# Kernel optimization log

Measured on AMD Instinct MI355X. Metric: run time of the kernel, lower is better.

The kernel has to match this reference:

```python
import jax, jax.numpy as jnp
import numpy as np
from jax import lax

# Model dims (see init_kwargs / mamba_ssm defaults)
B_, L_, D_IN = 8, 512, 128
D_MODEL, N_LAYERS = 512, 2
EXPAND, D_STATE, D_CONV = 2, 16, 4
D_INNER = EXPAND * D_MODEL          # 1024
DT_RANK = (D_MODEL + 15) // 16      # 32


def setup_inputs() -> dict:
    key = jax.random.key(0)
    ks = iter(jax.random.split(key, 32))
    def p(shape, scale=0.02):
        return jax.random.normal(next(ks), shape, jnp.float32) * scale
    inp = {}
    inp["x"] = jax.random.normal(next(ks), (B_, L_, D_IN), jnp.float32)
    # input projection (Linear(input_dim, d_model), with bias)
    inp["proj_in_w"] = p((D_MODEL, D_IN))
    inp["proj_in_b"] = p((D_MODEL,))
    # stacked per-layer Mamba params (leading dim = N_LAYERS)
    inp["in_proj_w"] = p((N_LAYERS, 2 * D_INNER, D_MODEL))      # no bias (mamba default)
    inp["conv_w"]    = p((N_LAYERS, D_INNER, D_CONV))           # depthwise conv1d
    inp["conv_b"]    = p((N_LAYERS, D_INNER))
    inp["x_proj_w"]  = p((N_LAYERS, DT_RANK + 2 * D_STATE, D_INNER))
    inp["dt_proj_w"] = p((N_LAYERS, D_INNER, DT_RANK))
    inp["dt_proj_b"] = jnp.full((N_LAYERS, D_INNER), 0.1, jnp.float32)
    inp["A_log"]     = jnp.log(jnp.tile(jnp.arange(1, D_STATE + 1, dtype=jnp.float32), (N_LAYERS, D_INNER, 1)))
    inp["Dm"]        = jnp.ones((N_LAYERS, D_INNER), jnp.float32)
    inp["out_proj_w"] = p((N_LAYERS, D_MODEL, D_INNER))         # no bias
    # classifier head: Linear(d_model, 64) -> ReLU -> Linear(64, 1)
    inp["cls_w1"] = p((64, D_MODEL)); inp["cls_b1"] = p((64,))
    inp["cls_w2"] = p((1, 64));       inp["cls_b2"] = p((1,))
    return inp


def _mamba_block(h, in_w, cw, cb, xp_w, dt_w, dt_b, A_log, Dm, out_w):
    B, L, _ = h.shape
    xz = jnp.einsum('bld,ed->ble', h, in_w)           # (B, L, 2*d_inner)
    xi, z = jnp.split(xz, 2, axis=-1)
    # causal depthwise conv1d (pad left d_conv-1, crop to L)
    xc = xi.transpose(0, 2, 1)                         # (B, d_inner, L)
    xc = lax.conv_general_dilated(
        xc, cw[:, None, :], (1,), [(D_CONV - 1, 0)],
        feature_group_count=D_INNER,
        dimension_numbers=('NCH', 'OIH', 'NCH')) + cb[None, :, None]
    xc = jax.nn.silu(xc).transpose(0, 2, 1)            # (B, L, d_inner)
    x_dbl = jnp.einsum('bld,ed->ble', xc, xp_w)        # (B, L, dt_rank + 2*d_state)
    dt, Bm, Cm = jnp.split(x_dbl, [DT_RANK, DT_RANK + D_STATE], axis=-1)
    dt = jax.nn.softplus(jnp.einsum('blr,dr->bld', dt, dt_w) + dt_b)  # (B, L, d_inner)
    A = -jnp.exp(A_log)                                # (d_inner, d_state)

    def step(hst, ins):
        dt_t, B_t, C_t, x_t = ins                      # (B,di),(B,ds),(B,ds),(B,di)
        dA = jnp.exp(dt_t[..., None] * A)              # (B, di, ds)
        hst = dA * hst + (dt_t * x_t)[..., None] * B_t[:, None, :]
        y = jnp.einsum('bds,bs->bd', hst, C_t)
        return hst, y

    h0 = jnp.zeros((B, D_INNER, D_STATE), h.dtype)
    xs = (dt.transpose(1, 0, 2), Bm.transpose(1, 0, 2),
          Cm.transpose(1, 0, 2), xc.transpose(1, 0, 2))
    _, ys = lax.scan(step, h0, xs)                     # ys: (L, B, d_inner)
    y = ys.transpose(1, 0, 2) + xc * Dm                # skip term D*x
    y = y * jax.nn.silu(z)                             # gate
    return jnp.einsum('ble,de->bld', y, out_w)         # (B, L, d_model)


def reference(x, proj_in_w, proj_in_b, in_proj_w, conv_w, conv_b, x_proj_w,
              dt_proj_w, dt_proj_b, A_log, Dm, out_proj_w,
              cls_w1, cls_b1, cls_w2, cls_b2):
    h = jnp.einsum('bli,di->bld', x, proj_in_w) + proj_in_b
    for l in range(N_LAYERS):
        h = _mamba_block(h, in_proj_w[l], conv_w[l], conv_b[l], x_proj_w[l],
                         dt_proj_w[l], dt_proj_b[l], A_log[l], Dm[l], out_proj_w[l])
    h = h.mean(axis=1)                                 # (B, d_model); dropout = identity (eval)
    h = jax.nn.relu(h @ cls_w1.T + cls_b1)
    logits = (h @ cls_w2.T + cls_b2).squeeze(-1)       # (B,)
    return logits
```

## Files before the change

kernel.cpp:

```cpp
#include <hip/hip_runtime.h>
#include <hip/hip_bf16.h>

#define B_   8
#define L_   512
#define DIN  128
#define DM   512
#define NLAY 2
#define DI   1024
#define DS   16
#define DTR  32
#define BL   (B_ * L_)
#define KS   8
#define CL   128
#define NCH  (L_ / CL)

typedef short bf16x8 __attribute__((ext_vector_type(8)));
typedef float floatx4 __attribute__((ext_vector_type(4)));

__device__ __forceinline__ unsigned short f2bf(float f) {
    unsigned int u = __float_as_uint(f);
    unsigned int r = (u + 0x7FFF + ((u >> 16) & 1)) >> 16;
    return (unsigned short)r;
}
__device__ __forceinline__ float bf2f(unsigned short u) {
    return __uint_as_float((unsigned int)u << 16);
}

#if __has_builtin(__builtin_amdgcn_exp2f)
#define EXP2(x) __builtin_amdgcn_exp2f(x)
#else
#define EXP2(x) __expf((x) * 0.69314718056f)
#endif

__device__ __forceinline__ void gld_lds16(const unsigned short* g, unsigned short* l) {
    __builtin_amdgcn_global_load_lds(
        (const __attribute__((address_space(1))) void*)g,
        (__attribute__((address_space(3))) void*)l,
        16, 0, 0);
}

__global__ __launch_bounds__(256) void cvt_all(
    const float* __restrict__ x,  unsigned short* __restrict__ xbf,
    const float* __restrict__ pw, unsigned short* __restrict__ wpin,
    const float* __restrict__ iw, unsigned short* __restrict__ win,
    const float* __restrict__ ow, unsigned short* __restrict__ wout,
    const float* __restrict__ dtp, unsigned short* __restrict__ dtwb,
    float* __restrict__ hm)
{
    int bid = blockIdx.x;
    if (bid >= 1856) {
        int i = (bid - 1856) * 2048 + threadIdx.x * 8;
        float4 z = make_float4(0.f, 0.f, 0.f, 0.f);
        *(float4*)(hm + i) = z;
        *(float4*)(hm + i + 4) = z;
        return;
    }
    const float* src; unsigned short* dst; int off;
    if      (bid < 256)  { src = x;   dst = xbf;  off = bid; }
    else if (bid < 288)  { src = pw;  dst = wpin; off = bid - 256; }
    else if (bid < 1312) { src = iw;  dst = win;  off = bid - 288; }
    else if (bid < 1824) { src = ow;  dst = wout; off = bid - 1312; }
    else                 { src = dtp; dst = dtwb; off = bid - 1824; }
    int i = (off * 256 + threadIdx.x) * 8;
    float4 a = *(const float4*)(src + i);
    float4 b = *(const float4*)(src + i + 4);
    unsigned short o[8];
    o[0] = f2bf(a.x); o[1] = f2bf(a.y); o[2] = f2bf(a.z); o[3] = f2bf(a.w);
    o[4] = f2bf(b.x); o[5] = f2bf(b.y); o[6] = f2bf(b.z); o[7] = f2bf(b.w);
    *(uint4*)(dst + i) = *(uint4*)o;
}

__global__ __launch_bounds__(256) void gemm_mfma(
    const unsigned short* __restrict__ A,
    const unsigned short* __restrict__ W,
    float* __restrict__ C, unsigned short* __restrict__ Cb,
    int N, int K)
{
    __shared__ unsigned short As[128 * 64];
    __shared__ unsigned short Ws[128 * 64];

    const int tid  = threadIdx.x;
    const int lane = tid & 63;
    const int wv   = tid >> 6;
    const int wm   = (wv >> 1) * 64;
    const int wn   = (wv & 1) * 64;
    const int lr   = lane & 15;
    const int q    = lane >> 4;

    const int srow  = lane >> 3;
    const int skcol = (lane & 7) * 8;
    const long aRowBase = (long)blockIdx.y * 128;
    const long wRowBase = (long)blockIdx.x * 128;

    floatx4 acc[4][4];
#pragma unroll
    for (int i = 0; i < 4; ++i)
#pragma unroll
        for (int j = 0; j < 4; ++j)
#pragma unroll
            for (int r = 0; r < 4; ++r) acc[i][j][r] = 0.f;

    for (int k0 = 0; k0 < K; k0 += 64) {
        __syncthreads();
#pragma unroll
        for (int c = 0; c < 4; ++c) {
            const int chunk = wv * 4 + c;
            const int row   = chunk * 8 + srow;
            gld_lds16(A + (aRowBase + row) * K + k0 + skcol,
                      As + chunk * 512 + lane * 8);
            gld_lds16(W + (wRowBase + row) * K + k0 + skcol,
                      Ws + chunk * 512 + lane * 8);
        }
        __syncthreads();

#pragma unroll
        for (int kk = 0; kk < 2; ++kk) {
            bf16x8 af[4], bfr[4];
#pragma unroll
            for (int i = 0; i < 4; ++i)
                af[i] = *(const bf16x8*)(As + (wm + i * 16 + lr) * 64 + kk * 32 + q * 8);
#pragma unroll
            for (int j = 0; j < 4; ++j)
                bfr[j] = *(const bf16x8*)(Ws + (wn + j * 16 + lr) * 64 + kk * 32 + q * 8);
#pragma unroll
            for (int i = 0; i < 4; ++i)
#pragma unroll
                for (int j = 0; j < 4; ++j)
                    acc[i][j] = __builtin_amdgcn_mfma_f32_16x16x32_bf16(
                        af[i], bfr[j], acc[i][j], 0, 0, 0);
        }
    }

#pragma unroll
    for (int i = 0; i < 4; ++i) {
#pragma unroll
        for (int r = 0; r < 4; ++r) {
            const int  crow = blockIdx.y * 128 + wm + i * 16 + q * 4 + r;
            const long base = (long)crow * N + blockIdx.x * 128 + wn + lr;
#pragma unroll
            for (int j = 0; j < 4; ++j) {
                float v = acc[i][j][r];
                if (C)  C[base + j * 16] = v;
                if (Cb) Cb[base + j * 16] = f2bf(v);
            }
        }
    }
}

__global__ __launch_bounds__(256) void gemm_mfma_n64(
    const unsigned short* __restrict__ A,
    const unsigned short* __restrict__ W,
    const float* __restrict__ bias,
    float* __restrict__ C, unsigned short* __restrict__ Cb,
    int N, int K, int meanmode, float* __restrict__ hm)
{
    __shared__ unsigned short As[128 * 64];
    __shared__ unsigned short Ws[64 * 64];
    __shared__ float colsum[64];

    const int tid  = threadIdx.x;
    const int lane = tid & 63;
    const int wv   = tid >> 6;
    const int wm   = wv * 32;
    const int lr   = lane & 15;
    const int q    = lane >> 4;

    const int srow  = lane >> 3;
    const int skcol = (lane & 7) * 8;
    const long aRowBase = (long)blockIdx.y * 128;
    const long wRowBase = (long)blockIdx.x * 64;

    floatx4 acc[2][4];
#pragma unroll
    for (int i = 0; i < 2; ++i)
#pragma unroll
        for (int j = 0; j < 4; ++j)
#pragma unroll
            for (int r = 0; r < 4; ++r) acc[i][j][r] = 0.f;

    for (int k0 = 0; k0 < K; k0 += 64) {
        __syncthreads();
#pragma unroll
        for (int c = 0; c < 4; ++c) {
            const int chunk = wv * 4 + c;
            const int row   = chunk * 8 + srow;
            gld_lds16(A + (aRowBase + row) * K + k0 + skcol,
                      As + chunk * 512 + lane * 8);
        }
#pragma unroll
        for (int c = 0; c < 2; ++c) {
            const int chunk = wv * 2 + c;
            const int row   = chunk * 8 + srow;
            gld_lds16(W + (wRowBase + row) * K + k0 + skcol,
                      Ws + chunk * 512 + lane * 8);
        }
        __syncthreads();

#pragma unroll
        for (int kk = 0; kk < 2; ++kk) {
            bf16x8 af[2], bfr[4];
#pragma unroll
            for (int i = 0; i < 2; ++i)
                af[i] = *(const bf16x8*)(As + (wm + i * 16 + lr) * 64 + kk * 32 + q * 8);
#pragma unroll
            for (int j = 0; j < 4; ++j)
                bfr[j] = *(const bf16x8*)(Ws + (j * 16 + lr) * 64 + kk * 32 + q * 8);
#pragma unroll
            for (int i = 0; i < 2; ++i)
#pragma unroll
                for (int j = 0; j < 4; ++j)
                    acc[i][j] = __builtin_amdgcn_mfma_f32_16x16x32_bf16(
                        af[i], bfr[j], acc[i][j], 0, 0, 0);
        }
    }

    if (meanmode) {
        if (tid < 64) colsum[tid] = 0.f;
        __syncthreads();
#pragma unroll
        for (int j = 0; j < 4; ++j) {
            float p = 0.f;
#pragma unroll
            for (int i = 0; i < 2; ++i)
#pragma unroll
                for (int r = 0; r < 4; ++r) p += acc[i][j][r];
            atomicAdd(&colsum[j * 16 + lr], p);
        }
        __syncthreads();
        if (tid < 64) {
            const int b = blockIdx.y >> 2;
            atomicAdd(&hm[b * DM + blockIdx.x * 64 + tid],
                      colsum[tid] * (1.f / (float)L_));
        }
        return;
    }

    float bj[4] = {0.f, 0.f, 0.f, 0.f};
    if (bias) {
#pragma unroll
        for (int j = 0; j < 4; ++j)
            bj[j] = bias[blockIdx.x * 64 + j * 16 + lr];
    }
#pragma unroll
    for (int i = 0; i < 2; ++i) {
#pragma unroll
        for (int r = 0; r < 4; ++r) {
            const int  crow = blockIdx.y * 128 + wm + i * 16 + q * 4 + r;
            const long base = (long)crow * N + blockIdx.x * 64 + lr;
#pragma unroll
            for (int j = 0; j < 4; ++j) {
                float v = acc[i][j][r] + bj[j];
                if (C)  C[base + j * 16] = v;
                if (Cb) Cb[base + j * 16] = f2bf(v);
            }
        }
    }
}

__global__ __launch_bounds__(256) void xprojconv(
    const unsigned short* __restrict__ xzb, const float* __restrict__ cw,
    const float* __restrict__ cb, const float* __restrict__ W,
    float* __restrict__ P, float* __restrict__ xcout)
{
    __shared__ float As[16][68];
    __shared__ float Ws[16][68];

    const int tid  = threadIdx.x;
    const int tx   = tid & 15;
    const int ty   = tid >> 4;
    const int lrow = tid >> 2;
    const int lk   = (tid & 3) << 2;
    const int kbase = blockIdx.x * (DI / KS);

    const int m = blockIdx.y * 64 + lrow;
    const int t = m & (L_ - 1);
    const float* Wp = W + lrow * DI + kbase + lk;

    float acc[4][4] = {};

    for (int k0 = 0; k0 < DI / KS; k0 += 16) {
        const int dcol = kbase + k0 + lk;
        float4 cbv = *(const float4*)(cb + dcol);
        float sums[4] = {cbv.x, cbv.y, cbv.z, cbv.w};
        float4 cwq[4];
#pragma unroll
        for (int q = 0; q < 4; ++q) cwq[q] = *(const float4*)(cw + (dcol + q) * 4);
#pragma unroll
        for (int w = 0; w < 4; ++w) {
            int tw = t - 3 + w;
            if (tw >= 0) {
                const uint2 up = *(const uint2*)(xzb + (long)(m - 3 + w) * (2 * DI) + dcol);
                float x0 = __uint_as_float(up.x << 16);
                float x1 = __uint_as_float(up.x & 0xffff0000u);
                float x2 = __uint_as_float(up.y << 16);
                float x3 = __uint_as_float(up.y & 0xffff0000u);
                sums[0] += ((const float*)&cwq[0])[w] * x0;
                sums[1] += ((const float*)&cwq[1])[w] * x1;
                sums[2] += ((const float*)&cwq[2])[w] * x2;
                sums[3] += ((const float*)&cwq[3])[w] * x3;
            }
        }
        float4 a4;
#pragma unroll
        for (int q = 0; q < 4; ++q)
            ((float*)&a4)[q] = sums[q] / (1.f + __expf(-sums[q]));
        float4 wv = *(const float4*)(Wp + k0);
        *(float4*)(xcout + (long)m * DI + dcol) = a4;

        __syncthreads();
        As[lk + 0][lrow] = a4.x; As[lk + 1][lrow] = a4.y;
        As[lk + 2][lrow] = a4.z; As[lk + 3][lrow] = a4.w;
        Ws[lk + 0][lrow] = wv.x; Ws[lk + 1][lrow] = wv.y;
        Ws[lk + 2][lrow] = wv.z; Ws[lk + 3][lrow] = wv.w;
        __syncthreads();
#pragma unroll
        for (int k = 0; k < 16; ++k) {
            const float4 a44 = *(const float4*)&As[k][ty << 2];
            const float4 w4  = *(const float4*)&Ws[k][tx << 2];
            acc[0][0] += a44.x * w4.x; acc[0][1] += a44.x * w4.y;
            acc[0][2] += a44.x * w4.z; acc[0][3] += a44.x * w4.w;
            acc[1][0] += a44.y * w4.x; acc[1][1] += a44.y * w4.y;
            acc[1][2] += a44.y * w4.z; acc[1][3] += a44.y * w4.w;
            acc[2][0] += a44.z * w4.x; acc[2][1] += a44.z * w4.y;
            acc[2][2] += a44.z * w4.z; acc[2][3] += a44.z * w4.w;
            acc[3][0] += a44.w * w4.x; acc[3][1] += a44.w * w4.y;
            acc[3][2] += a44.w * w4.z; acc[3][3] += a44.w * w4.w;
        }
    }

    float* out = P + (long)blockIdx.x * (BL * 64)
               + (blockIdx.y * 64 + (ty << 2)) * 64 + (tx << 2);
#pragma unroll
    for (int i = 0; i < 4; ++i)
        *(float4*)(out + i * 64) = make_float4(acc[i][0], acc[i][1],
                                               acc[i][2], acc[i][3]);
}

__global__ __launch_bounds__(256) void xproj_reduce(
    const float* __restrict__ P, float* __restrict__ xdbl,
    unsigned short* __restrict__ xdblb)
{
    int i = (blockIdx.x * 256 + threadIdx.x) * 4;
    float4 s = *(const float4*)(P + i);
#pragma unroll
    for (int k = 1; k < KS; ++k) {
        float4 p = *(const float4*)(P + (long)k * (BL * 64) + i);
        s.x += p.x; s.y += p.y; s.z += p.z; s.w += p.w;
    }
    *(float4*)(xdbl + i) = s;
    unsigned short o[4];
    o[0] = f2bf(s.x); o[1] = f2bf(s.y); o[2] = f2bf(s.z); o[3] = f2bf(s.w);
    *(uint2*)(xdblb + i) = *(uint2*)o;
}

template <int CTRL>
__device__ __forceinline__ float dpp_shr_add(float v) {
    int sh = __builtin_amdgcn_update_dpp(0, __float_as_int(v), CTRL, 0xF, 0xF, true);
    return v + __int_as_float(sh);
}

__global__ __launch_bounds__(256) void scan_fused(
    const float* __restrict__ xc, const float* __restrict__ xdbl,
    const unsigned short* __restrict__ xdblb,
    const unsigned short* __restrict__ dtwb,
    const float* __restrict__ dtpb,
    const float* __restrict__ A_log, const float* __restrict__ Dm,
    const unsigned short* __restrict__ xzb, unsigned short* __restrict__ ysb16)
{
    __shared__ float4 sdp [CL / 2][17];
    __shared__ float4 sbc4[CL / 2][17];
    __shared__ float  sy  [16][CL + 4];

    const int tid  = threadIdx.x;
    const int s    = tid & 15;
    const int grp  = tid >> 4;
    const int bd0  = blockIdx.x * 16;
    const int b    = bd0 >> 10;
    const int d0   = bd0 & (DI - 1);
    const int mb0  = b * L_;

    const int j    = tid & 15;
    const int tt   = tid >> 4;
    const int lane = tid & 63;
    const int w    = tid >> 6;
    const int q    = lane >> 4;
    const int tW   = 32 * w;

    const float a    = -__expf(A_log[(d0 + grp) * DS + s]);
    const float dmv  = Dm[d0 + j];
    const float bias = dtpb[d0 + j];

    const bf16x8 bfrag = *(const bf16x8*)(dtwb + (d0 + j) * 32 + q * 8);

    float  rB[8], rC[8];
    bf16x8 ra[2];
    float  rxc[2][4], rz[2][4];

#pragma unroll
    for (int i = 0; i < 8; ++i) {
        int m = mb0 + tt + 16 * i;
        rB[i] = xdbl[m * 64 + DTR + j];
        rC[i] = xdbl[m * 64 + DTR + DS + j];
    }
#pragma unroll
    for (int tile = 0; tile < 2; ++tile) {
        ra[tile] = *(const bf16x8*)(xdblb + (long)(mb0 + tW + tile * 16 + j) * 64 + q * 8);
#pragma unroll
        for (int r = 0; r < 4; ++r) {
            int t = tW + tile * 16 + q * 4 + r;
            rxc[tile][r] = xc[(mb0 + t) * DI + d0 + j];
            rz [tile][r] = bf2f(xzb[(long)(mb0 + t) * (2 * DI) + DI + d0 + j]);
        }
    }

    float state = 0.f;

    for (int c = 0; c < NCH; ++c) {
        const int mbase = mb0 + c * CL;
        float xcur[2][4], zcur[2][4];
#pragma unroll
        for (int tile = 0; tile < 2; ++tile)
#pragma unroll
            for (int r = 0; r < 4; ++r) {
                xcur[tile][r] = rxc[tile][r];
                zcur[tile][r] = rz[tile][r];
            }

        floatx4 dacc[2];
#pragma unroll
        for (int tile = 0; tile < 2; ++tile) {
            floatx4 cin;
            cin[0] = bias; cin[1] = bias; cin[2] = bias; cin[3] = bias;
            dacc[tile] = __builtin_amdgcn_mfma_f32_16x16x32_bf16(
                ra[tile], bfrag, cin, 0, 0, 0);
        }

        __syncthreads();
#pragma unroll
        for (int i = 0; i < 8; ++i) {
            int t = tt + 16 * i;
            ((float2*)&sbc4[t >> 1][j])[t & 1] = make_float2(rB[i], rC[i]);
        }
#pragma unroll
        for (int tile = 0; tile < 2; ++tile) {
#pragma unroll
            for (int r = 0; r < 4; ++r) {
                int t = tW + tile * 16 + q * 4 + r;
                float v = dacc[tile][r];
                float dt = (v > 20.f) ? v : __logf(1.f + __expf(v));
                ((float2*)&sdp[t >> 1][j])[t & 1] =
                    make_float2(dt * 1.44269504f, dt * xcur[tile][r]);
            }
        }
        __syncthreads();

        if (c < NCH - 1) {
            const int mn = mbase + CL;
#pragma unroll
            for (int i = 0; i < 8; ++i) {
                int m = mn + tt + 16 * i;
                rB[i] = xdbl[m * 64 + DTR + j];
                rC[i] = xdbl[m * 64 + DTR + DS + j];
            }
#pragma unroll
            for (int tile = 0; tile < 2; ++tile) {
                ra[tile] = *(const bf16x8*)(xdblb + (long)(mn + tW + tile * 16 + j) * 64 + q * 8);
#pragma unroll
                for (int r = 0; r < 4; ++r) {
                    int t = tW + tile * 16 + q * 4 + r;
                    rxc[tile][r] = xc[(mn + t) * DI + d0 + j];
                    rz [tile][r] = bf2f(xzb[(long)(mn + t) * (2 * DI) + DI + d0 + j]);
                }
            }
        }

        for (int t4 = 0; t4 < CL; t4 += 4) {
            float ybuf[4];
#pragma unroll
            for (int h = 0; h < 2; ++h) {
                const int t2 = (t4 >> 1) + h;
                const float4 dp = sdp[t2][grp];
                const float4 bc = sbc4[t2][s];
                {
                    const float dA = EXP2(dp.x * a);
                    state = fmaf(dA, state, dp.y * bc.x);
                    float contrib = state * bc.y;
                    contrib = dpp_shr_add<0x111>(contrib);
                    contrib = dpp_shr_add<0x112>(contrib);
                    contrib = dpp_shr_add<0x114>(contrib);
                    contrib = dpp_shr_add<0x118>(contrib);
                    ybuf[h * 2] = contrib;
                }
                {
                    const float dA = EXP2(dp.z * a);
                    state = fmaf(dA, state, dp.w * bc.z);
                    float contrib = state * bc.w;
                    contrib = dpp_shr_add<0x111>(contrib);
                    contrib = dpp_shr_add<0x112>(contrib);
                    contrib = dpp_shr_add<0x114>(contrib);
                    contrib = dpp_shr_add<0x118>(contrib);
                    ybuf[h * 2 + 1] = contrib;
                }
            }
            if (s == 15) *(float4*)&sy[grp][t4] = *(float4*)ybuf;
        }
        __syncthreads();

#pragma unroll
        for (int tile = 0; tile < 2; ++tile) {
#pragma unroll
            for (int r = 0; r < 4; ++r) {
                int t = tW + tile * 16 + q * 4 + r;
                float z = zcur[tile][r];
                float sz = z / (1.f + __expf(-z));
                float val = (sy[j][t] + xcur[tile][r] * dmv) * sz;
                ysb16[(long)(mbase + t) * DI + d0 + j] = f2bf(val);
            }
        }
    }
}

__global__ __launch_bounds__(512) void meancls_kernel(
    const float* __restrict__ hm, const float* __restrict__ w1,
    const float* __restrict__ b1, const float* __restrict__ w2,
    const float* __restrict__ b2, float* __restrict__ out)
{
    __shared__ float shm[DM];
    __shared__ float su[64];
    const int b = blockIdx.x, tid = threadIdx.x;
    shm[tid] = hm[b * DM + tid];
    __syncthreads();

    const int j = tid >> 3, sl = tid & 7;
    const float* wr = w1 + j * DM + sl * 64;
    const float* hb = shm + sl * 64;
    float p = 0.f;
    for (int k = 0; k < 64; k += 4)
        p += hb[k] * wr[k] + hb[k+1] * wr[k+1]
           + hb[k+2] * wr[k+2] + hb[k+3] * wr[k+3];
    p += __shfl_xor(p, 1);
    p += __shfl_xor(p, 2);
    p += __shfl_xor(p, 4);
    if (sl == 0) su[j] = fmaxf(p + b1[j], 0.f) * w2[j];
    __syncthreads();
    if (tid < 64) {
        float v = su[tid];
#pragma unroll
        for (int off = 32; off; off >>= 1) v += __shfl_down(v, off);
        if (tid == 0) out[b] = v + b2[0];
    }
}

extern "C" void kernel_launch(void* const* d_in, const int* in_sizes, int n_in,
                              void* d_out, int out_size, void* d_ws, size_t ws_size,
                              hipStream_t stream) {
    const float* x          = (const float*)d_in[0];
    const float* proj_in_w  = (const float*)d_in[1];
    const float* proj_in_b  = (const float*)d_in[2];
    const float* in_proj_w  = (const float*)d_in[3];
    const float* conv_w     = (const float*)d_in[4];
    const float* conv_b     = (const float*)d_in[5];
    const float* x_proj_w   = (const float*)d_in[6];
    const float* dt_proj_w  = (const float*)d_in[7];
    const float* dt_proj_b  = (const float*)d_in[8];
    const float* A_log      = (const float*)d_in[9];
    const float* Dm         = (const float*)d_in[10];
    const float* out_proj_w = (const float*)d_in[11];
    const float* cls_w1     = (const float*)d_in[12];
    const float* cls_b1     = (const float*)d_in[13];
    const float* cls_w2     = (const float*)d_in[14];
    const float* cls_b2     = (const float*)d_in[15];
    float* out = (float*)d_out;

    float* ws   = (float*)d_ws;
    float* h    = ws;
    float* xzf  = h    + BL * DM;
    float* xcb  = xzf  + BL * 2 * DI;
    float* xdbl = xcb  + BL * DI;
    float* scr  = xdbl + BL * 64;
    float* hm   = scr  + 2 * BL * DI;
    float* hmp  = hm   + B_ * DM;
    unsigned short* xzb  = (unsigned short*)xzf;
    unsigned short* u16  = (unsigned short*)(hmp + 64 * DM);
    unsigned short* xbf  = u16;
    unsigned short* hbf  = xbf  + BL * DIN;
    unsigned short* ysbf = hbf  + BL * DM;
    unsigned short* wpin = ysbf + BL * DI;
    unsigned short* win  = wpin + DM * DIN;
    unsigned short* wout = win  + NLAY * 2 * DI * DM;

    float* xpart = scr;
    unsigned short* xdblb = (unsigned short*)(scr + 6 * 1024 * 1024 + 262144);
    unsigned short* dtwb  = (unsigned short*)(scr + 6 * 1024 * 1024 + 262144 + 131072 + 16384);

    cvt_all<<<1858, 256, 0, stream>>>(x, xbf, proj_in_w, wpin,
                                      in_proj_w, win, out_proj_w, wout,
                                      dt_proj_w, dtwb, hm);

    gemm_mfma_n64<<<dim3(DM / 64, BL / 128), 256, 0, stream>>>(
        xbf, wpin, proj_in_b, nullptr, hbf, DM, DIN, 0, nullptr);

    for (int l = 0; l < NLAY; ++l) {
        gemm_mfma<<<dim3(2 * DI / 128, BL / 128), 256, 0, stream>>>(
            hbf, win + l * 2 * DI * DM, nullptr, xzb, 2 * DI, DM);
        xprojconv<<<dim3(KS, 64), 256, 0, stream>>>(
            xzb, conv_w + l * DI * 4, conv_b + l * DI,
            x_proj_w + l * 64 * DI, xpart, xcb);
        xproj_reduce<<<256, 256, 0, stream>>>(xpart, xdbl, xdblb);
        scan_fused<<<(B_ * DI) / 16, 256, 0, stream>>>(
            xcb, xdbl, xdblb, dtwb + l * DI * 32, dt_proj_b + l * DI,
            A_log + l * DI * DS, Dm + l * DI, xzb, ysbf);
        if (l == NLAY - 1) {
            gemm_mfma_n64<<<dim3(DM / 64, BL / 128), 256, 0, stream>>>(
                ysbf, wout + l * DM * DI, nullptr, nullptr, nullptr,
                DM, DI, 1, hm);
        } else {
            gemm_mfma_n64<<<dim3(DM / 64, BL / 128), 256, 0, stream>>>(
                ysbf, wout + l * DM * DI, nullptr, nullptr, hbf,
                DM, DI, 0, nullptr);
        }
    }

    meancls_kernel<<<B_, 512, 0, stream>>>(hm, cls_w1, cls_b1,
                                           cls_w2, cls_b2, out);
}
```

Before: 315.5 us.

## Replace split-K partial buffer and reduce kernel with atomic accumulation

The x_proj split-K kernel now accumulates its partial sums straight into a per-layer xdbl buffer with float atomicAdd, instead of writing eight partial slices that a separate reduce kernel then summed. The reduce kernel and its bf16 copy of xdbl are removed. The scan kernel now converts the fp32 xdbl values to bf16 as it loads them, and the conversion kernel gains extra blocks to zero both layers' xdbl buffers up front. This drops one launch and the large partial-sum round trip through memory, at the cost of atomic contention and a summation order that is no longer deterministic.

New measurement: 362.1 us. 1.15x slower.

```diff
diff --git a/kernel.cpp b/kernel.cpp
--- a/kernel.cpp
+++ b/kernel.cpp
@@ -39,15 +39,31 @@
         16, 0, 0);
 }
 
+__device__ __forceinline__ bf16x8 ldcvt_bf8(const float* __restrict__ p) {
+    float4 a = *(const float4*)p;
+    float4 b = *(const float4*)(p + 4);
+    unsigned short o[8];
+    o[0] = f2bf(a.x); o[1] = f2bf(a.y); o[2] = f2bf(a.z); o[3] = f2bf(a.w);
+    o[4] = f2bf(b.x); o[5] = f2bf(b.y); o[6] = f2bf(b.z); o[7] = f2bf(b.w);
+    return *(bf16x8*)o;
+}
+
 __global__ __launch_bounds__(256) void cvt_all(
     const float* __restrict__ x,  unsigned short* __restrict__ xbf,
     const float* __restrict__ pw, unsigned short* __restrict__ wpin,
     const float* __restrict__ iw, unsigned short* __restrict__ win,
     const float* __restrict__ ow, unsigned short* __restrict__ wout,
     const float* __restrict__ dtp, unsigned short* __restrict__ dtwb,
-    float* __restrict__ hm)
+    float* __restrict__ hm, float* __restrict__ xdblz)
 {
     int bid = blockIdx.x;
+    if (bid >= 1858) {
+        int i = (bid - 1858) * 2048 + threadIdx.x * 8;
+        float4 z = make_float4(0.f, 0.f, 0.f, 0.f);
+        *(float4*)(xdblz + i) = z;
+        *(float4*)(xdblz + i + 4) = z;
+        return;
+    }
     if (bid >= 1856) {
         int i = (bid - 1856) * 2048 + threadIdx.x * 8;
         float4 z = make_float4(0.f, 0.f, 0.f, 0.f);
@@ -260,7 +276,7 @@
 __global__ __launch_bounds__(256) void xprojconv(
     const unsigned short* __restrict__ xzb, const float* __restrict__ cw,
     const float* __restrict__ cb, const float* __restrict__ W,
-    float* __restrict__ P, float* __restrict__ xcout)
+    float* __restrict__ xdbl, float* __restrict__ xcout)
 {
     __shared__ float As[16][68];
     __shared__ float Ws[16][68];
@@ -328,29 +344,12 @@
         }
     }
 
-    float* out = P + (long)blockIdx.x * (BL * 64)
-               + (blockIdx.y * 64 + (ty << 2)) * 64 + (tx << 2);
+    float* outp = xdbl + (blockIdx.y * 64 + (ty << 2)) * 64 + (tx << 2);
 #pragma unroll
     for (int i = 0; i < 4; ++i)
-        *(float4*)(out + i * 64) = make_float4(acc[i][0], acc[i][1],
-                                               acc[i][2], acc[i][3]);
-}
-
-__global__ __launch_bounds__(256) void xproj_reduce(
-    const float* __restrict__ P, float* __restrict__ xdbl,
-    unsigned short* __restrict__ xdblb)
-{
-    int i = (blockIdx.x * 256 + threadIdx.x) * 4;
-    float4 s = *(const float4*)(P + i);
-#pragma unroll
-    for (int k = 1; k < KS; ++k) {
-        float4 p = *(const float4*)(P + (long)k * (BL * 64) + i);
-        s.x += p.x; s.y += p.y; s.z += p.z; s.w += p.w;
-    }
-    *(float4*)(xdbl + i) = s;
-    unsigned short o[4];
-    o[0] = f2bf(s.x); o[1] = f2bf(s.y); o[2] = f2bf(s.z); o[3] = f2bf(s.w);
-    *(uint2*)(xdblb + i) = *(uint2*)o;
+#pragma unroll
+        for (int k = 0; k < 4; ++k)
+            atomicAdd(&outp[i * 64 + k], acc[i][k]);
 }
 
 template <int CTRL>
@@ -361,7 +360,6 @@
 
 __global__ __launch_bounds__(256) void scan_fused(
     const float* __restrict__ xc, const float* __restrict__ xdbl,
-    const unsigned short* __restrict__ xdblb,
     const unsigned short* __restrict__ dtwb,
     const float* __restrict__ dtpb,
     const float* __restrict__ A_log, const float* __restrict__ Dm,
@@ -404,7 +402,7 @@
     }
 #pragma unroll
     for (int tile = 0; tile < 2; ++tile) {
-        ra[tile] = *(const bf16x8*)(xdblb + (long)(mb0 + tW + tile * 16 + j) * 64 + q * 8);
+        ra[tile] = ldcvt_bf8(xdbl + (long)(mb0 + tW + tile * 16 + j) * 64 + q * 8);
 #pragma unroll
         for (int r = 0; r < 4; ++r) {
             int t = tW + tile * 16 + q * 4 + r;
@@ -464,7 +462,7 @@
             }
 #pragma unroll
             for (int tile = 0; tile < 2; ++tile) {
-                ra[tile] = *(const bf16x8*)(xdblb + (long)(mn + tW + tile * 16 + j) * 64 + q * 8);
+                ra[tile] = ldcvt_bf8(xdbl + (long)(mn + tW + tile * 16 + j) * 64 + q * 8);
 #pragma unroll
                 for (int r = 0; r < 4; ++r) {
                     int t = tW + tile * 16 + q * 4 + r;
@@ -589,26 +587,24 @@
     unsigned short* win  = wpin + DM * DIN;
     unsigned short* wout = win  + NLAY * 2 * DI * DM;
 
-    float* xpart = scr;
-    unsigned short* xdblb = (unsigned short*)(scr + 6 * 1024 * 1024 + 262144);
-    unsigned short* dtwb  = (unsigned short*)(scr + 6 * 1024 * 1024 + 262144 + 131072 + 16384);
-
-    cvt_all<<<1858, 256, 0, stream>>>(x, xbf, proj_in_w, wpin,
+    unsigned short* dtwb = (unsigned short*)(scr + 6 * 1024 * 1024 + 262144 + 131072 + 16384);
+
+    cvt_all<<<2114, 256, 0, stream>>>(x, xbf, proj_in_w, wpin,
                                       in_proj_w, win, out_proj_w, wout,
-                                      dt_proj_w, dtwb, hm);
+                                      dt_proj_w, dtwb, hm, xdbl);
 
     gemm_mfma_n64<<<dim3(DM / 64, BL / 128), 256, 0, stream>>>(
         xbf, wpin, proj_in_b, nullptr, hbf, DM, DIN, 0, nullptr);
 
     for (int l = 0; l < NLAY; ++l) {
+        float* xdb_l = xdbl + (long)l * BL * 64;
         gemm_mfma<<<dim3(2 * DI / 128, BL / 128), 256, 0, stream>>>(
             hbf, win + l * 2 * DI * DM, nullptr, xzb, 2 * DI, DM);
         xprojconv<<<dim3(KS, 64), 256, 0, stream>>>(
             xzb, conv_w + l * DI * 4, conv_b + l * DI,
-            x_proj_w + l * 64 * DI, xpart, xcb);
-        xproj_reduce<<<256, 256, 0, stream>>>(xpart, xdbl, xdblb);
+            x_proj_w + l * 64 * DI, xdb_l, xcb);
         scan_fused<<<(B_ * DI) / 16, 256, 0, stream>>>(
-            xcb, xdbl, xdblb, dtwb + l * DI * 32, dt_proj_b + l * DI,
+            xcb, xdb_l, dtwb + l * DI * 32, dt_proj_b + l * DI,
             A_log + l * DI * DS, Dm + l * DI, xzb, ysbf);
         if (l == NLAY - 1) {
             gemm_mfma_n64<<<dim3(DM / 64, BL / 128), 256, 0, stream>>>(
```
